# Performance work log

Measured on AMD Instinct MI355X. Metric: run time of the kernel, lower is better.

## Reference

```python
import jax, jax.numpy as jnp
import numpy as np

N, M, D = 8192, 8192, 256
GAMMA = 1.0 / D  # standard RBF bandwidth gamma = 1/D


def setup_inputs() -> dict:
    key = jax.random.key(0)
    kx, ks = jax.random.split(key)
    x = jax.random.normal(kx, (N, D), dtype=jnp.float32)
    support = jax.random.normal(ks, (M, D), dtype=jnp.float32)
    return {"x": x, "support": support}


def reference(x, support):
    # Vectorized RBF Gram matrix: K[i, j] = exp(-gamma * ||x_i - s_j||^2)
    # ||x_i - s_j||^2 = ||x_i||^2 + ||s_j||^2 - 2 x_i . s_j  (cdist-style, one GEMM)
    x_sq = jnp.sum(x * x, axis=-1, keepdims=True)            # [N, 1]
    s_sq = jnp.sum(support * support, axis=-1)[None, :]      # [1, M]
    cross = jnp.einsum('nd,md->nm', x, support)              # [N, M]
    sq_dists = jnp.maximum(x_sq + s_sq - 2.0 * cross, 0.0)   # clamp fp error
    return jnp.exp(-GAMMA * sq_dists)
```

## Files before the change

### kernel.cpp

```cpp
#include <hip/hip_runtime.h>

#define N 8192
#define M 8192
#define D 256

typedef unsigned short ushort_t;
typedef __attribute__((ext_vector_type(8))) short short8;
typedef __attribute__((ext_vector_type(4))) float floatx4;

__device__ __forceinline__ unsigned short f2bf(float f) {
  unsigned int u = __float_as_uint(f);
  u += 0x7fffu + ((u >> 16) & 1u);
  return (unsigned short)(u >> 16);
}

__global__ __launch_bounds__(256) void prep_kernel(const float* __restrict__ x,
                                                   const float* __restrict__ s,
                                                   ushort_t* __restrict__ xb,
                                                   ushort_t* __restrict__ sb,
                                                   float* __restrict__ xn,
                                                   float* __restrict__ sn) {
  int gw = blockIdx.x * 4 + (threadIdx.x >> 6);
  int lane = threadIdx.x & 63;
  const float* src;
  ushort_t* dst;
  float* nrm;
  int row;
  if (gw < N) { src = x; dst = xb; nrm = xn; row = gw; }
  else        { src = s; dst = sb; nrm = sn; row = gw - N; }
  float4 v = ((const float4*)(src + (size_t)row * D))[lane];
  float ss = v.x * v.x + v.y * v.y + v.z * v.z + v.w * v.w;
  ushort4 o;
  o.x = f2bf(v.x); o.y = f2bf(v.y); o.z = f2bf(v.z); o.w = f2bf(v.w);
  int lr = row & 127;
  size_t off = (size_t)(row >> 7) * 65536 + (size_t)(lane >> 4) * 16384
             + (size_t)lr * 128
             + (size_t)(((((lane >> 1) & 7) ^ (lr & 7)) * 16) + (lane & 1) * 8);
  *(ushort4*)((char*)dst + off) = o;
#pragma unroll
  for (int offs = 32; offs > 0; offs >>= 1) ss += __shfl_down(ss, offs);
  if (lane == 0) nrm[row] = ss;
}

__device__ __forceinline__ void compute_round(const ushort_t* __restrict__ As,
                                              const ushort_t* __restrict__ Bs,
                                              floatx4 (&acc)[4][4], int wr, int wc,
                                              int q4, int m16) {
#pragma unroll
  for (int cc = 0; cc < 2; ++cc) {
    short8 a_frag[4], b_frag[4];
#pragma unroll
    for (int i = 0; i < 4; ++i) {
      const int row = wr + i * 16 + m16;
      a_frag[i] = *(const short8*)(As + row * 64 + (((cc * 4 + q4) ^ (row & 7)) << 3));
    }
#pragma unroll
    for (int j = 0; j < 4; ++j) {
      const int row = wc + j * 16 + m16;
      b_frag[j] = *(const short8*)(Bs + row * 64 + (((cc * 4 + q4) ^ (row & 7)) << 3));
    }
#pragma unroll
    for (int i = 0; i < 4; ++i)
#pragma unroll
      for (int j = 0; j < 4; ++j)
        acc[i][j] = __builtin_amdgcn_mfma_f32_16x16x32_bf16(a_frag[i], b_frag[j],
                                                            acc[i][j], 0, 0, 0);
  }
}

__device__ __forceinline__ void stage_round(const char* gA, const char* gB,
                                            char* lA, char* lB) {
#pragma unroll
  for (int i = 0; i < 4; ++i)
    __builtin_amdgcn_global_load_lds(
        (const __attribute__((address_space(1))) void*)(gA + i * 1024),
        (__attribute__((address_space(3))) void*)(lA + i * 1024), 16, 0, 0);
#pragma unroll
  for (int i = 0; i < 4; ++i)
    __builtin_amdgcn_global_load_lds(
        (const __attribute__((address_space(1))) void*)(gB + i * 1024),
        (__attribute__((address_space(3))) void*)(lB + i * 1024), 16, 0, 0);
}

__global__ __launch_bounds__(256, 2) void rbf_gemm(const ushort_t* __restrict__ X,
                                                   const ushort_t* __restrict__ S,
                                                   const float* __restrict__ xn,
                                                   const float* __restrict__ sn,
                                                   float* __restrict__ out) {
  __shared__ __attribute__((aligned(16))) ushort_t As[2][128 * 64];
  __shared__ __attribute__((aligned(16))) ushort_t Bs[2][128 * 64];
  __shared__ float nS[256];

  const int tid = threadIdx.x;
  const int lane = tid & 63;
  const int wave = tid >> 6;

  const int wg = blockIdx.y * 64 + blockIdx.x;
  const int swz = (wg & 7) * 512 + (wg >> 3);
  const int by = swz >> 6;
  const int bx = swz & 63;

  {
    const float* np = (tid < 128) ? (xn + by * 128 + tid)
                                  : (sn + bx * 128 + (tid - 128));
    nS[tid] = *np;
  }
  __builtin_amdgcn_sched_barrier(0);

  const char* gA = (const char*)X + (size_t)by * 65536 + wave * 4096 + lane * 16;
  const char* gB = (const char*)S + (size_t)bx * 65536 + wave * 4096 + lane * 16;
  char* lA0 = (char*)&As[0][0] + wave * 4096;
  char* lB0 = (char*)&Bs[0][0] + wave * 4096;
  char* lA1 = (char*)&As[1][0] + wave * 4096;
  char* lB1 = (char*)&Bs[1][0] + wave * 4096;

  const int wr = (wave >> 1) * 64;
  const int wc = (wave & 1) * 64;
  const int q4 = lane >> 4;
  const int m16 = lane & 15;

  floatx4 acc[4][4];
#pragma unroll
  for (int i = 0; i < 4; ++i)
#pragma unroll
    for (int j = 0; j < 4; ++j) acc[i][j] = (floatx4){0.f, 0.f, 0.f, 0.f};

  stage_round(gA, gB, lA0, lB0);

  stage_round(gA + 16384, gB + 16384, lA1, lB1);
  asm volatile("s_waitcnt vmcnt(8) lgkmcnt(0)" ::: "memory");
  __builtin_amdgcn_s_barrier();
  __builtin_amdgcn_sched_barrier(0);
  compute_round(As[0], Bs[0], acc, wr, wc, q4, m16);
  __builtin_amdgcn_s_barrier();

  stage_round(gA + 2 * 16384, gB + 2 * 16384, lA0, lB0);
  asm volatile("s_waitcnt vmcnt(8)" ::: "memory");
  __builtin_amdgcn_s_barrier();
  __builtin_amdgcn_sched_barrier(0);
  compute_round(As[1], Bs[1], acc, wr, wc, q4, m16);
  __builtin_amdgcn_s_barrier();

  stage_round(gA + 3 * 16384, gB + 3 * 16384, lA1, lB1);
  asm volatile("s_waitcnt vmcnt(8)" ::: "memory");
  __builtin_amdgcn_s_barrier();
  __builtin_amdgcn_sched_barrier(0);
  compute_round(As[0], Bs[0], acc, wr, wc, q4, m16);

  asm volatile("s_waitcnt vmcnt(0)" ::: "memory");
  __builtin_amdgcn_s_barrier();
  __builtin_amdgcn_sched_barrier(0);
  compute_round(As[1], Bs[1], acc, wr, wc, q4, m16);

  const float cexp = -1.0f / (float)D;
#pragma unroll
  for (int i = 0; i < 4; ++i) {
#pragma unroll
    for (int j = 0; j < 4; ++j) {
#pragma unroll
      for (int r = 0; r < 4; ++r) {
        const int rl = wr + i * 16 + q4 * 4 + r;
        const int cl = wc + j * 16 + m16;
        float sq = nS[rl] + nS[128 + cl] - 2.0f * acc[i][j][r];
        sq = fmaxf(sq, 0.0f);
        __builtin_nontemporal_store(
            __expf(cexp * sq),
            out + (size_t)(by * 128 + rl) * M + (bx * 128 + cl));
      }
    }
  }
}

extern "C" void kernel_launch(void* const* d_in, const int* in_sizes, int n_in,
                              void* d_out, int out_size, void* d_ws, size_t ws_size,
                              hipStream_t stream) {
  const float* x = (const float*)d_in[0];
  const float* s = (const float*)d_in[1];
  float* out = (float*)d_out;
  char* ws = (char*)d_ws;
  ushort_t* xb = (ushort_t*)ws;
  ushort_t* sb = (ushort_t*)(ws + (size_t)N * D * 2);
  float* xn = (float*)(ws + (size_t)(N + M) * D * 2);
  float* sn = xn + N;

  prep_kernel<<<(N + M) / 4, 256, 0, stream>>>(x, s, xb, sb, xn, sn);
  dim3 grid(M / 128, N / 128);
  rbf_gemm<<<grid, 256, 0, stream>>>(xb, sb, xn, sn, out);
}
```

Baseline: 317.8 us.

## Single-buffer LDS staging to fit three workgroups per CU and drop tile swizzle

Replaces the hand-scheduled double-buffered LDS pipeline with a single 32KB buffer. Each K round is now stage, sync, compute, with plain __syncthreads between them. Launch bounds rise to 3 waves-per-EU so more workgroups can be resident, and the aim is to hide latency through occupancy rather than explicit prefetch. The grouped workgroup index swizzle is also removed and plain blockIdx mapping is used. The risks are that loads no longer overlap compute within a workgroup, and that L2 locality may suffer without the swizzle.

```diff
diff --git a/kernel.cpp b/kernel.cpp
--- a/kernel.cpp
+++ b/kernel.cpp
@@ -82,37 +82,31 @@
         (__attribute__((address_space(3))) void*)(lB + i * 1024), 16, 0, 0);
 }
 
-__global__ __launch_bounds__(256, 2) void rbf_gemm(const ushort_t* __restrict__ X,
+__global__ __launch_bounds__(256, 3) void rbf_gemm(const ushort_t* __restrict__ X,
                                                    const ushort_t* __restrict__ S,
                                                    const float* __restrict__ xn,
                                                    const float* __restrict__ sn,
                                                    float* __restrict__ out) {
-  __shared__ __attribute__((aligned(16))) ushort_t As[2][128 * 64];
-  __shared__ __attribute__((aligned(16))) ushort_t Bs[2][128 * 64];
+  __shared__ __attribute__((aligned(16))) ushort_t As[128 * 64];
+  __shared__ __attribute__((aligned(16))) ushort_t Bs[128 * 64];
   __shared__ float nS[256];
 
   const int tid = threadIdx.x;
   const int lane = tid & 63;
   const int wave = tid >> 6;
-
-  const int wg = blockIdx.y * 64 + blockIdx.x;
-  const int swz = (wg & 7) * 512 + (wg >> 3);
-  const int by = swz >> 6;
-  const int bx = swz & 63;
+  const int bx = blockIdx.x;
+  const int by = blockIdx.y;
 
   {
     const float* np = (tid < 128) ? (xn + by * 128 + tid)
                                   : (sn + bx * 128 + (tid - 128));
     nS[tid] = *np;
   }
-  __builtin_amdgcn_sched_barrier(0);
 
   const char* gA = (const char*)X + (size_t)by * 65536 + wave * 4096 + lane * 16;
   const char* gB = (const char*)S + (size_t)bx * 65536 + wave * 4096 + lane * 16;
-  char* lA0 = (char*)&As[0][0] + wave * 4096;
-  char* lB0 = (char*)&Bs[0][0] + wave * 4096;
-  char* lA1 = (char*)&As[1][0] + wave * 4096;
-  char* lB1 = (char*)&Bs[1][0] + wave * 4096;
+  char* lA = (char*)As + wave * 4096;
+  char* lB = (char*)Bs + wave * 4096;
 
   const int wr = (wave >> 1) * 64;
   const int wc = (wave & 1) * 64;
@@ -125,32 +119,13 @@
 #pragma unroll
     for (int j = 0; j < 4; ++j) acc[i][j] = (floatx4){0.f, 0.f, 0.f, 0.f};
 
-  stage_round(gA, gB, lA0, lB0);
-
-  stage_round(gA + 16384, gB + 16384, lA1, lB1);
-  asm volatile("s_waitcnt vmcnt(8) lgkmcnt(0)" ::: "memory");
-  __builtin_amdgcn_s_barrier();
-  __builtin_amdgcn_sched_barrier(0);
-  compute_round(As[0], Bs[0], acc, wr, wc, q4, m16);
-  __builtin_amdgcn_s_barrier();
-
-  stage_round(gA + 2 * 16384, gB + 2 * 16384, lA0, lB0);
-  asm volatile("s_waitcnt vmcnt(8)" ::: "memory");
-  __builtin_amdgcn_s_barrier();
-  __builtin_amdgcn_sched_barrier(0);
-  compute_round(As[1], Bs[1], acc, wr, wc, q4, m16);
-  __builtin_amdgcn_s_barrier();
-
-  stage_round(gA + 3 * 16384, gB + 3 * 16384, lA1, lB1);
-  asm volatile("s_waitcnt vmcnt(8)" ::: "memory");
-  __builtin_amdgcn_s_barrier();
-  __builtin_amdgcn_sched_barrier(0);
-  compute_round(As[0], Bs[0], acc, wr, wc, q4, m16);
-
-  asm volatile("s_waitcnt vmcnt(0)" ::: "memory");
-  __builtin_amdgcn_s_barrier();
-  __builtin_amdgcn_sched_barrier(0);
-  compute_round(As[1], Bs[1], acc, wr, wc, q4, m16);
+#pragma unroll
+  for (int r = 0; r < 4; ++r) {
+    __syncthreads();
+    stage_round(gA + r * 16384, gB + r * 16384, lA, lB);
+    __syncthreads();
+    compute_round(As, Bs, acc, wr, wc, q4, m16);
+  }
 
   const float cexp = -1.0f / (float)D;
 #pragma unroll
```

Result: faster. 302.8 us (-4.7%).
